# Kernel optimization log

Measured on AMD Instinct MI355X. Metric: run time of the kernel, lower is better.

The kernel has to match this reference:

```python
import jax, jax.numpy as jnp
import numpy as np

NUM_SECTORS = 11


def setup_inputs() -> dict:
    key = jax.random.key(0)
    k0, k1, k2, k3 = jax.random.split(key, 4)
    B, N, C, H = 4, 2048, 512, 8
    x = jax.random.normal(k0, (B, N, C), dtype=jnp.float32)
    w_qkv = jax.random.normal(k1, (C, 3 * C), dtype=jnp.float32) * 0.02
    w_proj = jax.random.normal(k2, (C, C), dtype=jnp.float32) * 0.02
    b_proj = jnp.zeros((C,), dtype=jnp.float32)
    gate_logit = jnp.full((H,), 2.0, dtype=jnp.float32)
    sector_ids = jax.random.randint(k3, (N,), 0, NUM_SECTORS, dtype=jnp.int64)
    return {"x": x, "w_qkv": w_qkv, "w_proj": w_proj, "b_proj": b_proj,
            "gate_logit": gate_logit, "sector_ids": sector_ids}


def reference(x, w_qkv, w_proj, b_proj, gate_logit, sector_ids):
    B, N, C = x.shape
    H = gate_logit.shape[0]
    d = C // H
    scale = d ** -0.5

    qkv = (x @ w_qkv).reshape(B, N, 3, H, d)
    qkv = jnp.transpose(qkv, (2, 0, 3, 1, 4))  # (3, B, H, N, d)
    q, k, v = qkv[0], qkv[1], qkv[2]

    # Content attention: softmax(QK^T / sqrt(d)) @ V
    attn = jnp.einsum('bhnd,bhmd->bhnm', q, k) * scale
    attn = jax.nn.softmax(attn, axis=-1)
    v_content = jnp.einsum('bhnm,bhmd->bhnd', attn, v)

    # Positional path: A_pos @ V == per-sector mean of V, gathered per row.
    # A_pos[i,j] = 1/|sector(i)| if sector(i)==sector(j); row_sum >= 1 always.
    ids = sector_ids.astype(jnp.int32)
    counts = jax.ops.segment_sum(jnp.ones((N,), x.dtype), ids, num_segments=NUM_SECTORS)
    counts = jnp.maximum(counts, 1.0)
    v_nfirst = jnp.transpose(v, (2, 0, 1, 3)).reshape(N, B * H * d)  # (N, BHd)
    sums = jax.ops.segment_sum(v_nfirst, ids, num_segments=NUM_SECTORS)  # (S, BHd)
    means = sums / counts[:, None]
    v_pos = means[ids].reshape(N, B, H, d).transpose(1, 2, 0, 3)  # (B, H, N, d)

    g = jax.nn.sigmoid(gate_logit)[None, :, None, None]
    out = g * v_pos + (1.0 - g) * v_content  # (B, H, N, d)
    out = jnp.transpose(out, (0, 2, 1, 3)).reshape(B, N, C)
    return out @ w_proj + b_proj
```

## Files before the change

kernel.cpp:

```cpp
#include <hip/hip_runtime.h>
#include <hip/hip_bf16.h>
#include <stdint.h>

typedef float f32x4 __attribute__((ext_vector_type(4)));
typedef float f32x16 __attribute__((ext_vector_type(16)));
typedef short bf16x8 __attribute__((ext_vector_type(8)));
typedef short short4v __attribute__((ext_vector_type(4)));
typedef int i32x4 __attribute__((ext_vector_type(4)));

#define MFMA16(a, b, c) __builtin_amdgcn_mfma_f32_16x16x32_bf16(a, b, c, 0, 0, 0)
#define MFMA32(a, b, c) __builtin_amdgcn_mfma_f32_32x32x16_bf16(a, b, c, 0, 0, 0)

__device__ __forceinline__ float bf2f(unsigned short u) {
    unsigned int x = ((unsigned int)u) << 16;
    float f;
    __builtin_memcpy(&f, &x, 4);
    return f;
}
__device__ __forceinline__ unsigned short f2bf(float f) {
    unsigned int x;
    __builtin_memcpy(&x, &f, 4);
    unsigned int r = x + 0x7FFFu + ((x >> 16) & 1u);
    return (unsigned short)(r >> 16);
}
__device__ __forceinline__ unsigned int cvt_pk_bf16(float lo, float hi) {
    unsigned int d;
    asm("v_cvt_pk_bf16_f32 %0, %1, %2" : "=v"(d) : "v"(lo), "v"(hi));
    return d;
}

#define GLD16(g, l)                                                        \
    __builtin_amdgcn_global_load_lds(                                      \
        (const __attribute__((address_space(1))) void*)(g),                \
        (__attribute__((address_space(3))) void*)(l), 16, 0, 0)

#define QSCALE 0.18033688011112042f

__global__ __launch_bounds__(256) void k_cvt_x(const float* __restrict__ x,
                                               unsigned short* __restrict__ xb) {
    int i = (blockIdx.x * 256 + threadIdx.x) * 4;
    float4 v = *(const float4*)(x + i);
    short4v o;
    o.x = (short)f2bf(v.x);
    o.y = (short)f2bf(v.y);
    o.z = (short)f2bf(v.z);
    o.w = (short)f2bf(v.w);
    *(short4v*)(xb + i) = o;
}

__global__ __launch_bounds__(256) void k_transpose_bf16(const float* __restrict__ in,
                                                        unsigned short* __restrict__ out,
                                                        int R, int C) {
    __shared__ float tile[32][33];
    int tx = threadIdx.x & 31, ty = threadIdx.x >> 5;
    int r0 = blockIdx.y * 32, c0 = blockIdx.x * 32;
#pragma unroll
    for (int i = 0; i < 32; i += 8) tile[ty + i][tx] = in[(r0 + ty + i) * C + c0 + tx];
    __syncthreads();
#pragma unroll
    for (int i = 0; i < 32; i += 8) out[(c0 + ty + i) * R + r0 + tx] = f2bf(tile[tx][ty + i]);
}

__global__ __launch_bounds__(256) void k_gemm_qkv(const unsigned short* __restrict__ A,
                                                  const unsigned short* __restrict__ Bt,
                                                  unsigned short* __restrict__ Q,
                                                  unsigned short* __restrict__ Kd,
                                                  unsigned short* __restrict__ Vr) {
    __shared__ alignas(16) unsigned short As[128 * 64];
    __shared__ alignas(16) unsigned short Bs[128 * 64];
    const int t = threadIdx.x;
    const int w = t >> 6, l = t & 63;
    const int brow = blockIdx.x * 128, bcol = blockIdx.y * 128;
    const int wr = (w >> 1) * 64, wc = (w & 1) * 64;
    const int li = l & 15, lk = (l >> 4) * 8;
    f32x4 acc[4][4] = {};

    for (int kt = 0; kt < 512; kt += 64) {
#pragma unroll
        for (int i = 0; i < 4; i++) {
            int ub = i * 256 + w * 64;
            int r = (ub >> 3) + (l >> 3);
            int ck = l & 7;
            GLD16(A + (brow + r) * 512 + kt + ck * 8, As + ub * 8);
            GLD16(Bt + (bcol + r) * 512 + kt + ck * 8, Bs + ub * 8);
        }
        __syncthreads();
#pragma unroll
        for (int ks = 0; ks < 2; ks++) {
            bf16x8 af[4], bfr[4];
#pragma unroll
            for (int m = 0; m < 4; m++)
                af[m] = *(const bf16x8*)(As + (wr + m * 16 + li) * 64 + ks * 32 + lk);
#pragma unroll
            for (int n = 0; n < 4; n++)
                bfr[n] = *(const bf16x8*)(Bs + (wc + n * 16 + li) * 64 + ks * 32 + lk);
#pragma unroll
            for (int m = 0; m < 4; m++)
#pragma unroll
                for (int n = 0; n < 4; n++)
                    acc[m][n] = MFMA16(af[m], bfr[n], acc[m][n]);
        }
        __syncthreads();
    }
#pragma unroll
    for (int m = 0; m < 4; m++) {
#pragma unroll
        for (int n = 0; n < 4; n++) {
#pragma unroll
            for (int r = 0; r < 4; r++) {
                int gm = brow + wr + m * 16 + (l >> 4) * 4 + r;
                int gn = bcol + wc + n * 16 + li;
                float v = acc[m][n][r];
                int bb = gm >> 11, tok = gm & 2047;
                int three = gn >> 9, hh = (gn >> 6) & 7, dd = gn & 63;
                int bh = bb * 8 + hh;
                if (three == 0)
                    Q[((bh << 11) + tok) * 64 + dd] = f2bf(v * QSCALE);
                else if (three == 1)
                    Kd[((bh << 11) + tok) * 64 + dd] = f2bf(v);
                else
                    Vr[((bh << 11) + tok) * 64 + dd] = f2bf(v);
            }
        }
    }
}

__global__ __launch_bounds__(256) void k_transpose_v(const unsigned short* __restrict__ Vr,
                                                     unsigned short* __restrict__ Vt) {
    __shared__ unsigned short tile[64][68];
    int bh = blockIdx.x >> 5, nt = blockIdx.x & 31;
    int t = threadIdx.x;
    const unsigned short* src = Vr + ((size_t)bh * 2048 + nt * 64) * 64;
#pragma unroll
    for (int i = 0; i < 2; i++) {
        int row = i * 32 + (t >> 3);
        int col = (t & 7) * 8;
        *(bf16x8*)&tile[row][col] = *(const bf16x8*)(src + row * 64 + col);
    }
    __syncthreads();
    unsigned short* dst = Vt + (size_t)bh * 64 * 2048 + nt * 64;
#pragma unroll
    for (int i = 0; i < 2; i++) {
        int drow = i * 32 + (t >> 3);
        int ncol = (t & 7) * 8;
        bf16x8 v;
#pragma unroll
        for (int e = 0; e < 8; e++) v[e] = (short)tile[ncol + e][drow];
        *(bf16x8*)(dst + (size_t)drow * 2048 + ncol) = v;
    }
}

__global__ __launch_bounds__(256, 4) void k_attn(const unsigned short* __restrict__ Q,
                                                 const unsigned short* __restrict__ K,
                                                 const unsigned short* __restrict__ Vt,
                                                 float* __restrict__ vc) {
    __shared__ alignas(16) unsigned short Ks[2][64 * 64];
    __shared__ alignas(16) unsigned short Vs[2][64 * 64];
    const int bid = blockIdx.x;
    const int bh = bid >> 5, qb = bid & 31;
    const int w = threadIdx.x >> 6, l = threadIdx.x & 63;
    const int wq = w >> 1, wk = w & 1;
    const int q = l & 31, hi = l >> 5;
    const unsigned short* Qh = Q + (size_t)bh * 2048 * 64;
    const char* Kb = (const char*)(K + (size_t)bh * 2048 * 64);
    const char* Vb = (const char*)(Vt + (size_t)bh * 64 * 2048);
    const int qbase = qb * 64 + wq * 32;
    const int swz = (q & 7) << 4;

    bf16x8 qf[4];
#pragma unroll
    for (int ks = 0; ks < 4; ks++)
        qf[ks] = *(const bf16x8*)(Qh + (qbase + q) * 64 + ks * 16 + hi * 8);

    f32x16 o0 = {}, o1 = {};
    float mx = -1e30f, sm = 0.f;

    auto stage = [&](int buf, int kt) {
#pragma unroll
        for (int i = 0; i < 4; i++) {
            int idx = w * 4 + i;
            if (idx < 8) {
                int abase = idx * 1024;
                int al = abase + l * 16;
                int g = al ^ (((al >> 7) & 7) << 4);
                GLD16(Kb + (size_t)kt * 128 + g, (char*)Ks[buf] + abase);
            } else {
                int abase = (idx - 8) * 1024;
                int al = abase + l * 16;
                int row = al >> 7;
                int col = (al & 127) ^ ((row & 7) << 4);
                GLD16(Vb + (size_t)row * 4096 + kt * 2 + col, (char*)Vs[buf] + abase);
            }
        }
    };

    stage(0, 0);
    __syncthreads();

    for (int it = 0; it < 32; ++it) {
        const int cur = it & 1;
        if (it < 31) stage(cur ^ 1, (it + 1) * 64);

        const char* Kc = (const char*)Ks[cur];
        f32x16 s0 = {};
        __builtin_amdgcn_s_setprio(1);
#pragma unroll
        for (int ks = 0; ks < 4; ks++) {
            bf16x8 kf = *(const bf16x8*)(Kc + (wk * 32 + q) * 128 + ((ks * 32 + hi * 16) ^ swz));
            s0 = MFMA32(kf, qf[ks], s0);
        }
        __builtin_amdgcn_s_setprio(0);

        float c8[8];
#pragma unroll
        for (int r = 0; r < 8; r++) c8[r] = fmaxf(s0[r], s0[r + 8]);
#pragma unroll
        for (int r = 0; r < 4; r++) c8[r] = fmaxf(c8[r], c8[r + 4]);
        float tm = fmaxf(fmaxf(c8[0], c8[1]), fmaxf(c8[2], c8[3]));
        tm = fmaxf(tm, __shfl_xor(tm, 32));
        float mn = fmaxf(mx, tm);
        float fac = __builtin_amdgcn_exp2f(mx - mn);
        mx = mn;
#pragma unroll
        for (int r = 0; r < 16; r++) {
            o0[r] *= fac;
            o1[r] *= fac;
        }
        float a0 = 0.f, a1 = 0.f, a2 = 0.f, a3 = 0.f;
#pragma unroll
        for (int r = 0; r < 16; r += 4) {
            float p0 = __builtin_amdgcn_exp2f(s0[r] - mx);
            float p1 = __builtin_amdgcn_exp2f(s0[r + 1] - mx);
            float p2 = __builtin_amdgcn_exp2f(s0[r + 2] - mx);
            float p3 = __builtin_amdgcn_exp2f(s0[r + 3] - mx);
            s0[r] = p0;
            s0[r + 1] = p1;
            s0[r + 2] = p2;
            s0[r + 3] = p3;
            a0 += p0;
            a1 += p1;
            a2 += p2;
            a3 += p3;
        }
        float a = (a0 + a1) + (a2 + a3);
        a += __shfl_xor(a, 32);
        sm = sm * fac + a;

        unsigned int pk[4][2];
#pragma unroll
        for (int aa = 0; aa < 4; aa++)
#pragma unroll
            for (int c = 0; c < 2; c++)
                pk[aa][c] = cvt_pk_bf16(s0[4 * aa + 2 * c], s0[4 * aa + 2 * c + 1]);

        const char* Vc = (const char*)Vs[cur];
        __builtin_amdgcn_s_setprio(1);
#pragma unroll
        for (int ksl = 0; ksl < 2; ksl++) {
            unsigned int send0 = hi ? pk[2 * ksl][0] : pk[2 * ksl + 1][0];
            unsigned int send1 = hi ? pk[2 * ksl][1] : pk[2 * ksl + 1][1];
            unsigned int r0 = (unsigned int)__shfl_xor((int)send0, 32);
            unsigned int r1 = (unsigned int)__shfl_xor((int)send1, 32);
            unsigned int u0 = hi ? r0 : pk[2 * ksl][0];
            unsigned int u1 = hi ? r1 : pk[2 * ksl][1];
            unsigned int u2 = hi ? pk[2 * ksl + 1][0] : r0;
            unsigned int u3 = hi ? pk[2 * ksl + 1][1] : r1;
            i32x4 uu = {(int)u0, (int)u1, (int)u2, (int)u3};
            bf16x8 pa = __builtin_bit_cast(bf16x8, uu);
            int vcol = (wk * 64 + ksl * 32 + hi * 16);
            bf16x8 vf0 = *(const bf16x8*)(Vc + q * 128 + (vcol ^ swz));
            bf16x8 vf1 = *(const bf16x8*)(Vc + (q + 32) * 128 + (vcol ^ swz));
            o0 = MFMA32(pa, vf0, o0);
            o1 = MFMA32(pa, vf1, o1);
        }
        __builtin_amdgcn_s_setprio(0);

        __syncthreads();
    }

    float* So = ((float*)Ks) + wq * 2048;
    float* Sml = ((float*)Vs) + wq * 128;
    if (wk == 1) {
#pragma unroll
        for (int r = 0; r < 16; r++) {
            So[r * 64 + l] = o0[r];
            So[(16 + r) * 64 + l] = o1[r];
        }
        Sml[l] = mx;
        Sml[64 + l] = sm;
    }
    __syncthreads();
    if (wk == 0) {
        float m1 = Sml[l], l1 = Sml[64 + l];
        float ms = fmaxf(mx, m1);
        float f0 = __builtin_amdgcn_exp2f(mx - ms);
        float f1 = __builtin_amdgcn_exp2f(m1 - ms);
        float inv = 1.f / (f0 * sm + f1 * l1);
        float* vout = vc + ((size_t)bh * 2048 + qbase) * 64;
#pragma unroll
        for (int r = 0; r < 16; r++) {
            float om0 = f0 * o0[r] + f1 * So[r * 64 + l];
            float om1 = f0 * o1[r] + f1 * So[(16 + r) * 64 + l];
            int qq = (r & 3) + 8 * (r >> 2) + 4 * hi;
            float iv = __shfl(inv, qq);
            vout[qq * 64 + q] = om0 * iv;
            vout[qq * 64 + q + 32] = om1 * iv;
        }
    }
}

__global__ void k_counts(const int* __restrict__ ids, float* __restrict__ counts) {
    __shared__ float h[11];
    int t = threadIdx.x;
    if (t < 11) h[t] = 0.f;
    __syncthreads();
    for (int n = t; n < 2048; n += 256) atomicAdd(&h[ids[n]], 1.0f);
    __syncthreads();
    if (t < 11) counts[t] = h[t];
}

__global__ __launch_bounds__(256) void k_sums(const unsigned short* __restrict__ Vt,
                                              const int* __restrict__ ids,
                                              float* __restrict__ sums) {
    __shared__ int ids_s[512];
    int bh = blockIdx.x, ch = blockIdx.y;
    int t = threadIdx.x;
    ids_s[t] = ids[ch * 512 + t];
    ids_s[t + 256] = ids[ch * 512 + 256 + t];
    __syncthreads();
    int dd = t & 63, sub = t >> 6;
    const unsigned short* row = Vt + ((size_t)(bh * 64 + dd) << 11) + ch * 512 + sub * 128;
    const int* idp = ids_s + sub * 128;
    float acc[11] = {};
    for (int i = 0; i < 128; i++) {
        float v = bf2f(row[i]);
        int s = idp[i];
#pragma unroll
        for (int si = 0; si < 11; si++) acc[si] += (s == si) ? v : 0.f;
    }
#pragma unroll
    for (int si = 0; si < 11; si++) atomicAdd(&sums[((si * 32 + bh) << 6) + dd], acc[si]);
}

__global__ __launch_bounds__(256) void k_mix(const float* __restrict__ vc,
                                             const float* __restrict__ sums,
                                             const float* __restrict__ counts,
                                             const int* __restrict__ ids,
                                             const float* __restrict__ gate,
                                             unsigned short* __restrict__ mixb) {
    int tid = blockIdx.x * 256 + threadIdx.x;
    int m = tid >> 7;
    int c4 = (tid & 127) << 2;
    int b = m >> 11, tok = m & 2047;
    int h = c4 >> 6, dd = c4 & 63;
    int bh = b * 8 + h;
    int sid = ids[tok];
    float invc = 1.f / fmaxf(counts[sid], 1.f);
    float g = 1.f / (1.f + __expf(-gate[h]));
    float4 vp = *(const float4*)(sums + ((sid * 32 + bh) << 6) + dd);
    float4 vcv = *(const float4*)(vc + ((size_t)(bh << 11) + tok) * 64 + dd);
    short4v ov;
    ov.x = (short)f2bf(g * vp.x * invc + (1.f - g) * vcv.x);
    ov.y = (short)f2bf(g * vp.y * invc + (1.f - g) * vcv.y);
    ov.z = (short)f2bf(g * vp.z * invc + (1.f - g) * vcv.z);
    ov.w = (short)f2bf(g * vp.w * invc + (1.f - g) * vcv.w);
    *(short4v*)(mixb + (size_t)m * 512 + c4) = ov;
}

__global__ __launch_bounds__(256) void k_gemm_out(const unsigned short* __restrict__ A,
                                                  const unsigned short* __restrict__ Bt,
                                                  const float* __restrict__ bias,
                                                  float* __restrict__ out) {
    __shared__ alignas(16) unsigned short As[128 * 64];
    __shared__ alignas(16) unsigned short Bs[128 * 64];
    const int t = threadIdx.x;
    const int w = t >> 6, l = t & 63;
    const int brow = blockIdx.x * 128, bcol = blockIdx.y * 128;
    const int wr = (w >> 1) * 64, wc = (w & 1) * 64;
    const int li = l & 15, lk = (l >> 4) * 8;
    f32x4 acc[4][4] = {};

    for (int kt = 0; kt < 512; kt += 64) {
#pragma unroll
        for (int i = 0; i < 4; i++) {
            int ub = i * 256 + w * 64;
            int r = (ub >> 3) + (l >> 3);
            int ck = l & 7;
            GLD16(A + (brow + r) * 512 + kt + ck * 8, As + ub * 8);
            GLD16(Bt + (bcol + r) * 512 + kt + ck * 8, Bs + ub * 8);
        }
        __syncthreads();
#pragma unroll
        for (int ks = 0; ks < 2; ks++) {
            bf16x8 af[4], bfr[4];
#pragma unroll
            for (int m = 0; m < 4; m++)
                af[m] = *(const bf16x8*)(As + (wr + m * 16 + li) * 64 + ks * 32 + lk);
#pragma unroll
            for (int n = 0; n < 4; n++)
                bfr[n] = *(const bf16x8*)(Bs + (wc + n * 16 + li) * 64 + ks * 32 + lk);
#pragma unroll
            for (int m = 0; m < 4; m++)
#pragma unroll
                for (int n = 0; n < 4; n++)
                    acc[m][n] = MFMA16(af[m], bfr[n], acc[m][n]);
        }
        __syncthreads();
    }
#pragma unroll
    for (int m = 0; m < 4; m++) {
#pragma unroll
        for (int n = 0; n < 4; n++) {
#pragma unroll
            for (int r = 0; r < 4; r++) {
                int gm = brow + wr + m * 16 + (l >> 4) * 4 + r;
                int gn = bcol + wc + n * 16 + li;
                out[(size_t)gm * 512 + gn] = acc[m][n][r] + bias[gn];
            }
        }
    }
}

extern "C" void kernel_launch(void* const* d_in, const int* in_sizes, int n_in,
                              void* d_out, int out_size, void* d_ws, size_t ws_size,
                              hipStream_t stream) {
    const float* x = (const float*)d_in[0];
    const float* w_qkv = (const float*)d_in[1];
    const float* w_proj = (const float*)d_in[2];
    const float* b_proj = (const float*)d_in[3];
    const float* gate = (const float*)d_in[4];
    const int* ids = (const int*)d_in[5];
    float* out = (float*)d_out;
    char* ws = (char*)d_ws;

    unsigned short* xb = (unsigned short*)(ws + 0);
    unsigned short* wqT = (unsigned short*)(ws + 8388608);
    unsigned short* wpT = (unsigned short*)(ws + 9961472);
    unsigned short* Q = (unsigned short*)(ws + 10485760);
    unsigned short* Kd = (unsigned short*)(ws + 18874368);
    unsigned short* Vt = (unsigned short*)(ws + 27262976);
    float* vc = (float*)(ws + 35651584);
    unsigned short* Vrow = (unsigned short*)(ws + 35651584);
    float* sums = (float*)(ws + 52428800);
    float* counts = (float*)(ws + 52518912);
    unsigned short* mixb = xb;

    hipMemsetAsync(ws + 52428800, 0, 90112 + 64, stream);

    k_cvt_x<<<4096, 256, 0, stream>>>(x, xb);
    {
        dim3 g(48, 16);
        k_transpose_bf16<<<g, 256, 0, stream>>>(w_qkv, wqT, 512, 1536);
    }
    {
        dim3 g(16, 16);
        k_transpose_bf16<<<g, 256, 0, stream>>>(w_proj, wpT, 512, 512);
    }
    {
        dim3 g(64, 12);
        k_gemm_qkv<<<g, 256, 0, stream>>>(xb, wqT, Q, Kd, Vrow);
    }
    k_transpose_v<<<1024, 256, 0, stream>>>(Vrow, Vt);
    k_attn<<<1024, 256, 0, stream>>>(Q, Kd, Vt, vc);
    k_counts<<<1, 256, 0, stream>>>(ids, counts);
    {
        dim3 g(32, 4);
        k_sums<<<g, 256, 0, stream>>>(Vt, ids, sums);
    }
    k_mix<<<4096, 256, 0, stream>>>(vc, sums, counts, ids, gate, mixb);
    {
        dim3 g(64, 4);
        k_gemm_out<<<g, 256, 0, stream>>>(mixb, wpT, b_proj, out);
    }
}
```

Measured before the change: 215.8 us.

## Fuse gated sector-mean mix into attention epilogue and lazily rescale softmax

Removes the separate mix kernel and the fp32 content-attention buffer by computing the gated blend with per-sector means directly in the attention epilogue and writing bf16 output. The counts kernel now produces inverse counts, and the sums kernel runs before attention. Online softmax rescaling is skipped unless the tile max exceeds the running max by a threshold, and the row-sum cross-lane reduction is deferred to the end. The epilogue's stores are narrower and strided, and the lazy rescale allows unnormalized probabilities to grow before bf16 conversion.

```diff
diff --git a/kernel.cpp b/kernel.cpp
--- a/kernel.cpp
+++ b/kernel.cpp
@@ -153,7 +153,11 @@
 __global__ __launch_bounds__(256, 4) void k_attn(const unsigned short* __restrict__ Q,
                                                  const unsigned short* __restrict__ K,
                                                  const unsigned short* __restrict__ Vt,
-                                                 float* __restrict__ vc) {
+                                                 const float* __restrict__ sums,
+                                                 const float* __restrict__ invc,
+                                                 const int* __restrict__ ids,
+                                                 const float* __restrict__ gate,
+                                                 unsigned short* __restrict__ mixb) {
     __shared__ alignas(16) unsigned short Ks[2][64 * 64];
     __shared__ alignas(16) unsigned short Vs[2][64 * 64];
     const int bid = blockIdx.x;
@@ -217,15 +221,20 @@
 #pragma unroll
         for (int r = 0; r < 4; r++) c8[r] = fmaxf(c8[r], c8[r + 4]);
         float tm = fmaxf(fmaxf(c8[0], c8[1]), fmaxf(c8[2], c8[3]));
-        tm = fmaxf(tm, __shfl_xor(tm, 32));
-        float mn = fmaxf(mx, tm);
-        float fac = __builtin_amdgcn_exp2f(mx - mn);
-        mx = mn;
-#pragma unroll
-        for (int r = 0; r < 16; r++) {
-            o0[r] *= fac;
-            o1[r] *= fac;
-        }
+
+        if (!__all(tm <= mx + 8.0f)) {
+            float tmf = fmaxf(tm, __shfl_xor(tm, 32));
+            float mn = fmaxf(mx, tmf);
+            float fac = __builtin_amdgcn_exp2f(mx - mn);
+            mx = mn;
+#pragma unroll
+            for (int r = 0; r < 16; r++) {
+                o0[r] *= fac;
+                o1[r] *= fac;
+            }
+            sm *= fac;
+        }
+
         float a0 = 0.f, a1 = 0.f, a2 = 0.f, a3 = 0.f;
 #pragma unroll
         for (int r = 0; r < 16; r += 4) {
@@ -242,9 +251,7 @@
             a2 += p2;
             a3 += p3;
         }
-        float a = (a0 + a1) + (a2 + a3);
-        a += __shfl_xor(a, 32);
-        sm = sm * fac + a;
+        sm += (a0 + a1) + (a2 + a3);
 
         unsigned int pk[4][2];
 #pragma unroll
@@ -278,6 +285,8 @@
         __syncthreads();
     }
 
+    sm = sm + __shfl_xor(sm, 32);
+
     float* So = ((float*)Ks) + wq * 2048;
     float* Sml = ((float*)Vs) + wq * 128;
     if (wk == 1) {
@@ -296,27 +305,34 @@
         float f0 = __builtin_amdgcn_exp2f(mx - ms);
         float f1 = __builtin_amdgcn_exp2f(m1 - ms);
         float inv = 1.f / (f0 * sm + f1 * l1);
-        float* vout = vc + ((size_t)bh * 2048 + qbase) * 64;
+        float g = 1.f / (1.f + __expf(-gate[bh & 7]));
+        float omg = 1.f - g;
+        unsigned short* mrow = mixb + (size_t)(bh >> 3) * 2048 * 512 + (bh & 7) * 64;
 #pragma unroll
         for (int r = 0; r < 16; r++) {
             float om0 = f0 * o0[r] + f1 * So[r * 64 + l];
             float om1 = f0 * o1[r] + f1 * So[(16 + r) * 64 + l];
             int qq = (r & 3) + 8 * (r >> 2) + 4 * hi;
             float iv = __shfl(inv, qq);
-            vout[qq * 64 + q] = om0 * iv;
-            vout[qq * 64 + q + 32] = om1 * iv;
-        }
-    }
-}
-
-__global__ void k_counts(const int* __restrict__ ids, float* __restrict__ counts) {
+            int tok = qbase + qq;
+            int sid = ids[tok];
+            float ic = invc[sid];
+            float vp0 = sums[((sid * 32 + bh) << 6) + q];
+            float vp1 = sums[((sid * 32 + bh) << 6) + q + 32];
+            mrow[(size_t)tok * 512 + q] = f2bf(g * vp0 * ic + omg * om0 * iv);
+            mrow[(size_t)tok * 512 + q + 32] = f2bf(g * vp1 * ic + omg * om1 * iv);
+        }
+    }
+}
+
+__global__ void k_counts(const int* __restrict__ ids, float* __restrict__ invc) {
     __shared__ float h[11];
     int t = threadIdx.x;
     if (t < 11) h[t] = 0.f;
     __syncthreads();
     for (int n = t; n < 2048; n += 256) atomicAdd(&h[ids[n]], 1.0f);
     __syncthreads();
-    if (t < 11) counts[t] = h[t];
+    if (t < 11) invc[t] = 1.f / fmaxf(h[t], 1.f);
 }
 
 __global__ __launch_bounds__(256) void k_sums(const unsigned short* __restrict__ Vt,
@@ -340,31 +356,6 @@
     }
 #pragma unroll
     for (int si = 0; si < 11; si++) atomicAdd(&sums[((si * 32 + bh) << 6) + dd], acc[si]);
-}
-
-__global__ __launch_bounds__(256) void k_mix(const float* __restrict__ vc,
-                                             const float* __restrict__ sums,
-                                             const float* __restrict__ counts,
-                                             const int* __restrict__ ids,
-                                             const float* __restrict__ gate,
-                                             unsigned short* __restrict__ mixb) {
-    int tid = blockIdx.x * 256 + threadIdx.x;
-    int m = tid >> 7;
-    int c4 = (tid & 127) << 2;
-    int b = m >> 11, tok = m & 2047;
-    int h = c4 >> 6, dd = c4 & 63;
-    int bh = b * 8 + h;
-    int sid = ids[tok];
-    float invc = 1.f / fmaxf(counts[sid], 1.f);
-    float g = 1.f / (1.f + __expf(-gate[h]));
-    float4 vp = *(const float4*)(sums + ((sid * 32 + bh) << 6) + dd);
-    float4 vcv = *(const float4*)(vc + ((size_t)(bh << 11) + tok) * 64 + dd);
-    short4v ov;
-    ov.x = (short)f2bf(g * vp.x * invc + (1.f - g) * vcv.x);
-    ov.y = (short)f2bf(g * vp.y * invc + (1.f - g) * vcv.y);
-    ov.z = (short)f2bf(g * vp.z * invc + (1.f - g) * vcv.z);
-    ov.w = (short)f2bf(g * vp.w * invc + (1.f - g) * vcv.w);
-    *(short4v*)(mixb + (size_t)m * 512 + c4) = ov;
 }
 
 __global__ __launch_bounds__(256) void k_gemm_out(const unsigned short* __restrict__ A,
@@ -439,10 +430,9 @@
     unsigned short* Q = (unsigned short*)(ws + 10485760);
     unsigned short* Kd = (unsigned short*)(ws + 18874368);
     unsigned short* Vt = (unsigned short*)(ws + 27262976);
-    float* vc = (float*)(ws + 35651584);
     unsigned short* Vrow = (unsigned short*)(ws + 35651584);
     float* sums = (float*)(ws + 52428800);
-    float* counts = (float*)(ws + 52518912);
+    float* invc = (float*)(ws + 52518912);
     unsigned short* mixb = xb;
 
     hipMemsetAsync(ws + 52428800, 0, 90112 + 64, stream);
@@ -461,13 +451,12 @@
         k_gemm_qkv<<<g, 256, 0, stream>>>(xb, wqT, Q, Kd, Vrow);
     }
     k_transpose_v<<<1024, 256, 0, stream>>>(Vrow, Vt);
-    k_attn<<<1024, 256, 0, stream>>>(Q, Kd, Vt, vc);
-    k_counts<<<1, 256, 0, stream>>>(ids, counts);
+    k_counts<<<1, 256, 0, stream>>>(ids, invc);
     {
         dim3 g(32, 4);
         k_sums<<<g, 256, 0, stream>>>(Vt, ids, sums);
     }
-    k_mix<<<4096, 256, 0, stream>>>(vc, sums, counts, ids, gate, mixb);
+    k_attn<<<1024, 256, 0, stream>>>(Q, Kd, Vt, sums, invc, ids, gate, mixb);
     {
         dim3 g(64, 4);
         k_gemm_out<<<g, 256, 0, stream>>>(mixb, wpT, b_proj, out);
```

Measured after the change: 207.3 us. 3.9% less time.
